# Performance work log

Measured on AMD Instinct MI355X. Metric: run time of the kernel, lower is better.

## Reference

```python
import jax, jax.numpy as jnp
import numpy as np

N_HEAD = 16
N_EMBED = 2048


def setup_inputs() -> dict:
    key = jax.random.key(0)
    k1, k2, k3, k4, k5 = jax.random.split(key, 5)
    B, T, C = 4, 2048, N_EMBED
    scale = 1.0 / np.sqrt(C)
    return {
        "x": jax.random.normal(k1, (B, T, C), dtype=jnp.float32),
        "w_attn": jax.random.normal(k2, (C, 3 * C), dtype=jnp.float32) * scale,
        "b_attn": jnp.zeros((3 * C,), dtype=jnp.float32),
        "w_proj": jax.random.normal(k3, (C, C), dtype=jnp.float32) * scale,
        "b_proj": jnp.zeros((C,), dtype=jnp.float32),
    }


def reference(x, w_attn, b_attn, w_proj, b_proj):
    B, T, C = x.shape
    H = N_HEAD
    hd = C // H
    # fused QKV projection: [B,T,3C]
    qkv = jnp.einsum("btc,cd->btd", x, w_attn) + b_attn
    q, k, v = jnp.split(qkv, 3, axis=-1)
    # [B,H,T,hd]
    q = q.reshape(B, T, H, hd).transpose(0, 2, 1, 3)
    k = k.reshape(B, T, H, hd).transpose(0, 2, 1, 3)
    v = v.reshape(B, T, H, hd).transpose(0, 2, 1, 3)
    # scaled dot-product attention (no mask, no dropout at eval)
    scores = jnp.einsum("bhqd,bhkd->bhqk", q, k) / jnp.sqrt(jnp.asarray(hd, dtype=q.dtype))
    attn = jax.nn.softmax(scores, axis=-1)
    y = jnp.einsum("bhqk,bhkd->bhqd", attn, v)
    y = y.transpose(0, 2, 1, 3).reshape(B, T, C)
    return jnp.einsum("btc,cd->btd", y, w_proj) + b_proj
```

## Files before the change

kernel.cpp:

```cpp
#include <hip/hip_runtime.h>
#include <hip/hip_fp16.h>

typedef _Float16 f16;
typedef _Float16 half8 __attribute__((ext_vector_type(8)));
typedef _Float16 half4v __attribute__((ext_vector_type(4)));
typedef float f32x4 __attribute__((ext_vector_type(4)));

#define NBAT 4
#define NT   2048
#define NC   2048
#define NHEAD 16
#define HD   128
#define NM   8192
#define N3C  6144
#define QK_LD 4096
#define ATT_SCALE 0.088388347648318447f

static __device__ __forceinline__ void gload16(const void* g, void* l) {
  __builtin_amdgcn_global_load_lds(
      (const __attribute__((address_space(1))) unsigned int*)g,
      (__attribute__((address_space(3))) unsigned int*)l, 16, 0, 0);
}


__global__ __launch_bounds__(256) void cvt_x_f16(const float* __restrict__ in,
                                                 f16* __restrict__ out) {
  size_t i = ((size_t)blockIdx.x * 256 + threadIdx.x) * 8;
  float4 a = *(const float4*)(in + i);
  float4 b = *(const float4*)(in + i + 4);
  half8 o;
  o[0] = (f16)a.x; o[1] = (f16)a.y; o[2] = (f16)a.z; o[3] = (f16)a.w;
  o[4] = (f16)b.x; o[5] = (f16)b.y; o[6] = (f16)b.z; o[7] = (f16)b.w;
  *(half8*)(out + i) = o;
}

__global__ __launch_bounds__(256) void cvt_tr_f16(const float* __restrict__ in,
                                                  f16* __restrict__ out,
                                                  int R, int CC) {
  __shared__ float tile[32][33];
  int cb = blockIdx.x * 32, rb = blockIdx.y * 32;
  int lx = threadIdx.x & 31, ly = threadIdx.x >> 5;
  for (int i = 0; i < 32; i += 8)
    tile[ly + i][lx] = in[(size_t)(rb + ly + i) * CC + cb + lx];
  __syncthreads();
  for (int i = 0; i < 32; i += 8)
    out[(size_t)(cb + ly + i) * R + rb + lx] = (f16)tile[lx][ly + i];
}

template <int OUTMODE>
__global__ __launch_bounds__(512, 2)
void gemm256(const f16* __restrict__ A, const f16* __restrict__ BT,
             const float* __restrict__ bias,
             f16* __restrict__ oqk, f16* __restrict__ ovT,
             float* __restrict__ of32, int N, int K, int nbn) {
  __shared__ f16 sA[4 * 8192];
  __shared__ f16 sB[4 * 8192];

  const int tid = threadIdx.x;
  const int wv = tid >> 6, lane = tid & 63;
  const int lr = lane & 15, lg = lane >> 4;
  const int wm = wv >> 2, wn = wv & 3;

  const int bid = blockIdx.x;
  const int xcd = bid & 7, li = bid >> 3;
  const int bm = (xcd & 3) * 8 + (li & 7);
  const int bn = (xcd >> 2) * (nbn >> 1) + (li >> 3);

  const int q0 = tid >> 3;
  const int cx = (tid & 7) ^ (q0 & 7);
  const f16* aSrc = A + (size_t)(bm * 256 + q0) * K + cx * 8;
  const f16* bSrc = BT + (size_t)(bn * 256 + q0) * K + cx * 8;
  const size_t rs64 = (size_t)64 * K, rs128 = (size_t)128 * K;

  const int NKT = K >> 6, NIT = NKT >> 1;
  f32x4 acc[8][4] = {};

  auto stgA = [&](int t, int h, int bu) {
    const f16* s = aSrc + (size_t)h * rs128 + t * 64;
    f16* d = sA + (bu * 2 + h) * 8192 + tid * 8;
    gload16(s, d);
    gload16(s + rs64, d + 4096);
  };
  auto stgB = [&](int t, int h, int bu) {
    const f16* s = bSrc + (size_t)h * rs128 + t * 64;
    f16* d = sB + (bu * 2 + h) * 8192 + tid * 8;
    gload16(s, d);
    gload16(s + rs64, d + 4096);
  };

  stgA(0, 0, 0); stgA(0, 1, 0);
  stgB(0, 0, 0); stgB(0, 1, 0);
  stgB(1, 0, 1); stgB(1, 1, 1);
  asm volatile("s_waitcnt vmcnt(4)" ::: "memory");
  __builtin_amdgcn_s_barrier();
  asm volatile("" ::: "memory");

  const int xcs[2] = {((0 * 4 + lg) ^ (lr & 7)) * 8, ((1 * 4 + lg) ^ (lr & 7)) * 8};

  for (int it = 0; it < NIT; ++it) {
    const int u = 2 * it, v = u + 1;
    const bool notlast = (it < NIT - 1);
    half8 bfrag[4][2];
#pragma unroll
    for (int p = 0; p < 8; ++p) {
      const int buf = (p < 4) ? 0 : 1;
      const f16* bA = sA + (buf * 2 + wm) * 8192;
      const f16* bB = sB + (buf * 2 + (wn >> 1)) * 8192;
      const int mf0 = (p & 3) * 2;
      if ((p & 3) == 0) {
#pragma unroll
        for (int nf = 0; nf < 4; ++nf)
#pragma unroll
          for (int ks = 0; ks < 2; ++ks)
            bfrag[nf][ks] = *(const half8*)(
                bB + ((wn & 1) * 64 + nf * 16 + lr) * 64 + xcs[ks]);
      }
      half8 afrag[2][2];
#pragma unroll
      for (int m2 = 0; m2 < 2; ++m2)
#pragma unroll
        for (int ks = 0; ks < 2; ++ks)
          afrag[m2][ks] = *(const half8*)(
              bA + ((mf0 + m2) * 16 + lr) * 64 + xcs[ks]);
      switch (p) {
        case 0: stgA(v, 0, 1); break;
        case 1: stgA(v, 1, 1); break;
        case 2: if (notlast) stgB(u + 2, 0, 0); break;
        case 3: if (notlast) stgB(u + 2, 1, 0); break;
        case 4: if (notlast) stgA(u + 2, 0, 0); break;
        case 5: if (notlast) stgA(u + 2, 1, 0); break;
        case 6: if (notlast) stgB(v + 2, 0, 1); break;
        case 7: if (notlast) stgB(v + 2, 1, 1); break;
      }
      if ((p & 3) == 3) {
        if (notlast) asm volatile("s_waitcnt vmcnt(4)" ::: "memory");
        else         asm volatile("s_waitcnt vmcnt(0)" ::: "memory");
      }
      asm volatile("" ::: "memory");
      __builtin_amdgcn_s_barrier();
      asm volatile("" ::: "memory");
      __builtin_amdgcn_s_setprio(1);
#pragma unroll
      for (int m2 = 0; m2 < 2; ++m2)
#pragma unroll
        for (int nf = 0; nf < 4; ++nf)
#pragma unroll
          for (int ks = 0; ks < 2; ++ks)
            acc[mf0 + m2][nf] = __builtin_amdgcn_mfma_f32_16x16x32_f16(
                afrag[m2][ks], bfrag[nf][ks], acc[mf0 + m2][nf], 0, 0, 0);
      __builtin_amdgcn_s_setprio(0);
      asm volatile("" ::: "memory");
      __builtin_amdgcn_s_barrier();
    }
  }

#pragma unroll
  for (int nf = 0; nf < 4; ++nf) {
    const int col = bn * 256 + wn * 64 + nf * 16 + lr;
    const float bv = bias[col];
#pragma unroll
    for (int mf = 0; mf < 8; ++mf) {
      const int row0 = bm * 256 + wm * 128 + mf * 16 + lg * 4;
      f32x4 v = acc[mf][nf];
      if (OUTMODE == 0) {
#pragma unroll
        for (int r = 0; r < 4; ++r)
          of32[(size_t)(row0 + r) * N + col] = v[r] + bv;
      } else {
        if (col < 4096) {
          const float sc = (col < 2048) ? ATT_SCALE : 1.0f;
#pragma unroll
          for (int r = 0; r < 4; ++r)
            oqk[(size_t)(row0 + r) * QK_LD + col] = (f16)((v[r] + bv) * sc);
        } else {
          const int dfull = col - 4096;
          const int hh = dfull >> 7, dd = dfull & 127;
          const int bb = row0 >> 11, tt0 = row0 & 2047;
          half4v pk;
#pragma unroll
          for (int r = 0; r < 4; ++r) pk[r] = (f16)(v[r] + bv);
          *(half4v*)(ovT + ((size_t)(bb * NHEAD + hh) * HD + dd) * NT + tt0) = pk;
        }
      }
    }
  }
}

__global__ __launch_bounds__(256, 2)
void attn_fwd(const f16* __restrict__ qk, const f16* __restrict__ vT,
              f16* __restrict__ y) {
  const int bid = blockIdx.x;
  const int sid = (bid & 7) * 128 + (bid >> 3);
  const int qt = sid & 15;
  const int bh = sid >> 4;
  const int b = bh >> 4, h = bh & 15;
  const int tid = threadIdx.x, w = tid >> 6, lane = tid & 63;
  const int lr = lane & 15, lg = lane >> 4;

  __shared__ f16 Ks[2][64 * 128];
  __shared__ f16 Vs[2][128 * 64];
  __shared__ f16 Ps[4][2][16 * 64];

  half8 qf[2][4];
  for (int s = 0; s < 2; ++s) {
    const f16* qp = qk + (size_t)(b * NT + qt * 128 + w * 32 + s * 16 + lr) * QK_LD +
                    h * HD + lg * 8;
    for (int dc = 0; dc < 4; ++dc) qf[s][dc] = *(const half8*)(qp + dc * 32);
  }

  f32x4 accy[2][8] = {};
  f32x4 lacc[2] = {};
  float mrow[2][4];
  for (int s = 0; s < 2; ++s)
    for (int r = 0; r < 4; ++r) mrow[s][r] = -1e30f;

  half8 onev;
  for (int j = 0; j < 8; ++j) onev[j] = (f16)1.0f;

  const char* kbase[4];
  const char* vbase[4];
  for (int j = 0; j < 4; ++j) {
    int idx = w * 4 + j;
    {
      int row = idx * 4 + lg;
      int swz = (lr * 16) ^ ((row & 7) << 4);
      kbase[j] = (const char*)qk +
                 ((size_t)(b * NT + row) * QK_LD + 2048 + h * HD) * 2 + swz;
    }
    {
      int d = idx * 8 + (lane >> 3);
      int cj = (lane & 7) ^ (d & 7);
      vbase[j] = (const char*)vT + ((size_t)(bh * HD + d) * NT + cj * 8) * 2;
    }
  }

  for (int j = 0; j < 4; ++j) {
    int idx = w * 4 + j;
    gload16(kbase[j], (void*)((char*)Ks[0] + idx * 1024));
    gload16(vbase[j], (void*)((char*)Vs[0] + idx * 1024));
  }

  int cur = 0;
  for (int kt = 0; kt < 32; ++kt) {
    if (kt + 1 < 32) {
      for (int j = 0; j < 4; ++j) {
        int idx = w * 4 + j;
        gload16(kbase[j] + (size_t)(kt + 1) * (64 * QK_LD * 2),
                (void*)((char*)Ks[cur ^ 1] + idx * 1024));
        gload16(vbase[j] + (size_t)(kt + 1) * 128,
                (void*)((char*)Vs[cur ^ 1] + idx * 1024));
      }
    }
    if (kt < 31) asm volatile("s_waitcnt vmcnt(8)" ::: "memory");
    else         asm volatile("s_waitcnt vmcnt(0)" ::: "memory");
    __builtin_amdgcn_s_barrier();
    asm volatile("" ::: "memory");

    f32x4 sa[2][4] = {};
    for (int nb = 0; nb < 4; ++nb) {
      int kvr = nb * 16 + lr;
      const char* kr = (const char*)Ks[cur] + kvr * 256;
      int s7 = (kvr & 7) << 4;
      for (int dc = 0; dc < 4; ++dc) {
        half8 kb = *(const half8*)(kr + ((dc * 64 + lg * 16) ^ s7));
        sa[0][nb] = __builtin_amdgcn_mfma_f32_16x16x32_f16(qf[0][dc], kb, sa[0][nb], 0, 0, 0);
        sa[1][nb] = __builtin_amdgcn_mfma_f32_16x16x32_f16(qf[1][dc], kb, sa[1][nb], 0, 0, 0);
      }
    }

    for (int s = 0; s < 2; ++s) {
      float pml[4] = {-1e30f, -1e30f, -1e30f, -1e30f};
      for (int nb = 0; nb < 4; ++nb)
        for (int r = 0; r < 4; ++r)
          pml[r] = fmaxf(pml[r], sa[s][nb][r]);
      bool ok = true;
      for (int r = 0; r < 4; ++r) ok &= (pml[r] <= mrow[s][r] + 8.0f);
      if (!__all(ok)) {
        for (int r = 0; r < 4; ++r) {
          for (int off = 1; off < 16; off <<= 1)
            pml[r] = fmaxf(pml[r], __shfl_xor(pml[r], off));
          float mn = fmaxf(mrow[s][r], pml[r]);
          float al = __expf(mrow[s][r] - mn);
          mrow[s][r] = mn;
          lacc[s][r] *= al;
          for (int db = 0; db < 8; ++db) accy[s][db][r] *= al;
        }
      }
      for (int nb = 0; nb < 4; ++nb)
        for (int r = 0; r < 4; ++r) {
          float p = __expf(sa[s][nb][r] - mrow[s][r]);
          int prow = lg * 4 + r;
          int chunk = (nb * 2 + (lr >> 3)) ^ (prow & 7);
          Ps[w][s][prow * 64 + chunk * 8 + (lr & 7)] = (f16)p;
        }
    }

    half8 pa[2][2];
    for (int s = 0; s < 2; ++s)
      for (int kc = 0; kc < 2; ++kc) {
        int chunk = (kc * 4 + lg) ^ (lr & 7);
        pa[s][kc] = *(const half8*)(&Ps[w][s][lr * 64 + chunk * 8]);
      }
    for (int s = 0; s < 2; ++s)
      for (int kc = 0; kc < 2; ++kc)
        lacc[s] = __builtin_amdgcn_mfma_f32_16x16x32_f16(pa[s][kc], onev, lacc[s], 0, 0, 0);

    for (int db = 0; db < 8; ++db) {
      int d = db * 16 + lr;
      const char* vr = (const char*)Vs[cur] + d * 128;
      int d7 = d & 7;
      for (int kc = 0; kc < 2; ++kc) {
        half8 vb = *(const half8*)(vr + (((kc * 4 + lg) ^ d7) * 16));
        accy[0][db] = __builtin_amdgcn_mfma_f32_16x16x32_f16(pa[0][kc], vb, accy[0][db], 0, 0, 0);
        accy[1][db] = __builtin_amdgcn_mfma_f32_16x16x32_f16(pa[1][kc], vb, accy[1][db], 0, 0, 0);
      }
    }

    asm volatile("" ::: "memory");
    __builtin_amdgcn_s_barrier();
    cur ^= 1;
  }

  for (int s = 0; s < 2; ++s) {
    f32x4 inv;
    for (int r = 0; r < 4; ++r) inv[r] = 1.0f / lacc[s][r];
    f16* yp = y + (size_t)(b * NT + qt * 128 + w * 32 + s * 16 + lg * 4) * NC +
              h * HD + lr;
    for (int db = 0; db < 8; ++db)
      for (int r = 0; r < 4; ++r)
        yp[(size_t)r * NC + db * 16] = (f16)(accy[s][db][r] * inv[r]);
  }
}

extern "C" void kernel_launch(void* const* d_in, const int* in_sizes, int n_in,
                              void* d_out, int out_size, void* d_ws, size_t ws_size,
                              hipStream_t stream) {
  (void)in_sizes; (void)n_in; (void)out_size; (void)ws_size;
  const float* x      = (const float*)d_in[0];
  const float* w_attn = (const float*)d_in[1];
  const float* b_attn = (const float*)d_in[2];
  const float* w_proj = (const float*)d_in[3];
  const float* b_proj = (const float*)d_in[4];
  float* out = (float*)d_out;

  char* p = (char*)d_ws;
  f16* xh  = (f16*)p; p += (size_t)NM * NC * 2;
  f16* waT = (f16*)p; p += (size_t)N3C * NC * 2;
  f16* wpT = (f16*)p; p += (size_t)NC * NC * 2;
  f16* qkb = (f16*)p; p += (size_t)NM * QK_LD * 2;
  f16* vT  = (f16*)p; p += (size_t)NBAT * NHEAD * HD * NT * 2;
  f16* yh  = (f16*)p; p += (size_t)NM * NC * 2;

  cvt_x_f16<<<8192, 256, 0, stream>>>(x, xh);
  cvt_tr_f16<<<dim3(192, 64), 256, 0, stream>>>(w_attn, waT, NC, N3C);
  cvt_tr_f16<<<dim3(64, 64), 256, 0, stream>>>(w_proj, wpT, NC, NC);
  gemm256<1><<<768, 512, 0, stream>>>(xh, waT, b_attn, qkb, vT, nullptr,
                                      N3C, NC, 24);
  attn_fwd<<<1024, 256, 0, stream>>>(qkb, vT, yh);
  gemm256<0><<<256, 512, 0, stream>>>(yh, wpT, b_proj, nullptr, nullptr,
                                      out, NC, NC, 8);
}
```

Baseline: 472.8 us.

## Double-buffer LDS fragment reads in GEMM and reorder attention MFMA loops

The GEMM main loop is rewritten so that LDS reads for the next A/B fragment group are issued into a second register set while the MFMAs for the current group run. This hides LDS latency behind matrix math. Launch bounds are relaxed to one block per CU to make room for the extra fragment registers, which may cost occupancy. The attention kernel's QK and PV loops are reordered so the k-chunk index is outermost, interleaving independent accumulator chains.

```diff
diff --git a/kernel.cpp b/kernel.cpp
--- a/kernel.cpp
+++ b/kernel.cpp
@@ -48,7 +48,7 @@
 }
 
 template <int OUTMODE>
-__global__ __launch_bounds__(512, 2)
+__global__ __launch_bounds__(512, 1)
 void gemm256(const f16* __restrict__ A, const f16* __restrict__ BT,
              const float* __restrict__ bias,
              f16* __restrict__ oqk, f16* __restrict__ ovT,
@@ -96,63 +96,99 @@
   asm volatile("" ::: "memory");
 
   const int xcs[2] = {((0 * 4 + lg) ^ (lr & 7)) * 8, ((1 * 4 + lg) ^ (lr & 7)) * 8};
+  const f16* bAbase = sA + wm * 8192;
+  const f16* bBbase = sB + (wn >> 1) * 8192 + ((wn & 1) * 64 + lr) * 64;
+
+  half8 af0[2][2], af1[2][2];
+  half8 bf0[4][2], bf1[4][2];
+
+#define RD_A(DST, BUF, MQ)                                                  \
+  {                                                                         \
+    const f16* _pa = bAbase + (BUF)*16384;                                  \
+    _Pragma("unroll") for (int m2 = 0; m2 < 2; ++m2)                        \
+      _Pragma("unroll") for (int ks = 0; ks < 2; ++ks)                      \
+        DST[m2][ks] = *(const half8*)(_pa + (((MQ) + m2) * 16 + lr) * 64 +  \
+                                      xcs[ks]);                             \
+  }
+#define RD_B(DST, BUF)                                                      \
+  {                                                                         \
+    const f16* _pb = bBbase + (BUF)*16384;                                  \
+    _Pragma("unroll") for (int nf = 0; nf < 4; ++nf)                        \
+      _Pragma("unroll") for (int ks = 0; ks < 2; ++ks)                      \
+        DST[nf][ks] = *(const half8*)(_pb + nf * 16 * 64 + xcs[ks]);        \
+  }
+#define MFMA16(AF, BF, MF0)                                                 \
+  __builtin_amdgcn_s_setprio(1);                                            \
+  _Pragma("unroll") for (int ks = 0; ks < 2; ++ks)                          \
+    _Pragma("unroll") for (int m2 = 0; m2 < 2; ++m2)                        \
+      _Pragma("unroll") for (int nf = 0; nf < 4; ++nf)                      \
+        acc[(MF0) + m2][nf] = __builtin_amdgcn_mfma_f32_16x16x32_f16(       \
+            AF[m2][ks], BF[nf][ks], acc[(MF0) + m2][nf], 0, 0, 0);          \
+  __builtin_amdgcn_s_setprio(0);
+#define BAR1 asm volatile("" ::: "memory"); __builtin_amdgcn_s_barrier(); \
+             asm volatile("" ::: "memory");
+#define BAR2 asm volatile("" ::: "memory"); __builtin_amdgcn_s_barrier();
+
+  RD_A(af0, 0, 0);
+  RD_B(bf0, 0);
 
   for (int it = 0; it < NIT; ++it) {
     const int u = 2 * it, v = u + 1;
     const bool notlast = (it < NIT - 1);
-    half8 bfrag[4][2];
-#pragma unroll
-    for (int p = 0; p < 8; ++p) {
-      const int buf = (p < 4) ? 0 : 1;
-      const f16* bA = sA + (buf * 2 + wm) * 8192;
-      const f16* bB = sB + (buf * 2 + (wn >> 1)) * 8192;
-      const int mf0 = (p & 3) * 2;
-      if ((p & 3) == 0) {
-#pragma unroll
-        for (int nf = 0; nf < 4; ++nf)
-#pragma unroll
-          for (int ks = 0; ks < 2; ++ks)
-            bfrag[nf][ks] = *(const half8*)(
-                bB + ((wn & 1) * 64 + nf * 16 + lr) * 64 + xcs[ks]);
-      }
-      half8 afrag[2][2];
-#pragma unroll
-      for (int m2 = 0; m2 < 2; ++m2)
-#pragma unroll
-        for (int ks = 0; ks < 2; ++ks)
-          afrag[m2][ks] = *(const half8*)(
-              bA + ((mf0 + m2) * 16 + lr) * 64 + xcs[ks]);
-      switch (p) {
-        case 0: stgA(v, 0, 1); break;
-        case 1: stgA(v, 1, 1); break;
-        case 2: if (notlast) stgB(u + 2, 0, 0); break;
-        case 3: if (notlast) stgB(u + 2, 1, 0); break;
-        case 4: if (notlast) stgA(u + 2, 0, 0); break;
-        case 5: if (notlast) stgA(u + 2, 1, 0); break;
-        case 6: if (notlast) stgB(v + 2, 0, 1); break;
-        case 7: if (notlast) stgB(v + 2, 1, 1); break;
-      }
-      if ((p & 3) == 3) {
-        if (notlast) asm volatile("s_waitcnt vmcnt(4)" ::: "memory");
-        else         asm volatile("s_waitcnt vmcnt(0)" ::: "memory");
-      }
-      asm volatile("" ::: "memory");
-      __builtin_amdgcn_s_barrier();
-      asm volatile("" ::: "memory");
-      __builtin_amdgcn_s_setprio(1);
-#pragma unroll
-      for (int m2 = 0; m2 < 2; ++m2)
-#pragma unroll
-        for (int nf = 0; nf < 4; ++nf)
-#pragma unroll
-          for (int ks = 0; ks < 2; ++ks)
-            acc[mf0 + m2][nf] = __builtin_amdgcn_mfma_f32_16x16x32_f16(
-                afrag[m2][ks], bfrag[nf][ks], acc[mf0 + m2][nf], 0, 0, 0);
-      __builtin_amdgcn_s_setprio(0);
-      asm volatile("" ::: "memory");
-      __builtin_amdgcn_s_barrier();
-    }
-  }
+    stgA(v, 0, 1);
+    BAR1;
+    RD_A(af1, 0, 2);
+    MFMA16(af0, bf0, 0);
+    BAR2;
+    stgA(v, 1, 1);
+    BAR1;
+    RD_A(af0, 0, 4);
+    MFMA16(af1, bf0, 2);
+    BAR2;
+    if (notlast) stgB(u + 2, 0, 0);
+    BAR1;
+    RD_A(af1, 0, 6);
+    MFMA16(af0, bf0, 4);
+    BAR2;
+    if (notlast) stgB(u + 2, 1, 0);
+    if (notlast) { asm volatile("s_waitcnt vmcnt(4)" ::: "memory"); }
+    else         { asm volatile("s_waitcnt vmcnt(0)" ::: "memory"); }
+    BAR1;
+    RD_A(af0, 1, 0);
+    RD_B(bf1, 1);
+    MFMA16(af1, bf0, 6);
+    BAR2;
+    if (notlast) stgA(u + 2, 0, 0);
+    BAR1;
+    RD_A(af1, 1, 2);
+    MFMA16(af0, bf1, 0);
+    BAR2;
+    if (notlast) stgA(u + 2, 1, 0);
+    BAR1;
+    RD_A(af0, 1, 4);
+    MFMA16(af1, bf1, 2);
+    BAR2;
+    if (notlast) stgB(v + 2, 0, 1);
+    BAR1;
+    RD_A(af1, 1, 6);
+    MFMA16(af0, bf1, 4);
+    BAR2;
+    if (notlast) stgB(v + 2, 1, 1);
+    if (notlast) { asm volatile("s_waitcnt vmcnt(4)" ::: "memory"); }
+    else         { asm volatile("s_waitcnt vmcnt(0)" ::: "memory"); }
+    BAR1;
+    if (notlast) {
+      RD_A(af0, 0, 0);
+      RD_B(bf0, 0);
+    }
+    MFMA16(af1, bf1, 6);
+    BAR2;
+  }
+#undef RD_A
+#undef RD_B
+#undef MFMA16
+#undef BAR1
+#undef BAR2
 
 #pragma unroll
   for (int nf = 0; nf < 4; ++nf) {
@@ -161,24 +197,24 @@
 #pragma unroll
     for (int mf = 0; mf < 8; ++mf) {
       const int row0 = bm * 256 + wm * 128 + mf * 16 + lg * 4;
-      f32x4 v = acc[mf][nf];
+      f32x4 vv = acc[mf][nf];
       if (OUTMODE == 0) {
 #pragma unroll
         for (int r = 0; r < 4; ++r)
-          of32[(size_t)(row0 + r) * N + col] = v[r] + bv;
+          of32[(size_t)(row0 + r) * N + col] = vv[r] + bv;
       } else {
         if (col < 4096) {
           const float sc = (col < 2048) ? ATT_SCALE : 1.0f;
 #pragma unroll
           for (int r = 0; r < 4; ++r)
-            oqk[(size_t)(row0 + r) * QK_LD + col] = (f16)((v[r] + bv) * sc);
+            oqk[(size_t)(row0 + r) * QK_LD + col] = (f16)((vv[r] + bv) * sc);
         } else {
           const int dfull = col - 4096;
           const int hh = dfull >> 7, dd = dfull & 127;
           const int bb = row0 >> 11, tt0 = row0 & 2047;
           half4v pk;
 #pragma unroll
-          for (int r = 0; r < 4; ++r) pk[r] = (f16)(v[r] + bv);
+          for (int r = 0; r < 4; ++r) pk[r] = (f16)(vv[r] + bv);
           *(half4v*)(ovT + ((size_t)(bb * NHEAD + hh) * HD + dd) * NT + tt0) = pk;
         }
       }
@@ -257,11 +293,13 @@
     asm volatile("" ::: "memory");
 
     f32x4 sa[2][4] = {};
-    for (int nb = 0; nb < 4; ++nb) {
-      int kvr = nb * 16 + lr;
-      const char* kr = (const char*)Ks[cur] + kvr * 256;
-      int s7 = (kvr & 7) << 4;
-      for (int dc = 0; dc < 4; ++dc) {
+#pragma unroll
+    for (int dc = 0; dc < 4; ++dc) {
+#pragma unroll
+      for (int nb = 0; nb < 4; ++nb) {
+        int kvr = nb * 16 + lr;
+        const char* kr = (const char*)Ks[cur] + kvr * 256;
+        int s7 = (kvr & 7) << 4;
         half8 kb = *(const half8*)(kr + ((dc * 64 + lg * 16) ^ s7));
         sa[0][nb] = __builtin_amdgcn_mfma_f32_16x16x32_f16(qf[0][dc], kb, sa[0][nb], 0, 0, 0);
         sa[1][nb] = __builtin_amdgcn_mfma_f32_16x16x32_f16(qf[1][dc], kb, sa[1][nb], 0, 0, 0);
@@ -301,15 +339,19 @@
         int chunk = (kc * 4 + lg) ^ (lr & 7);
         pa[s][kc] = *(const half8*)(&Ps[w][s][lr * 64 + chunk * 8]);
       }
-    for (int s = 0; s < 2; ++s)
-      for (int kc = 0; kc < 2; ++kc)
+#pragma unroll
+    for (int kc = 0; kc < 2; ++kc)
+#pragma unroll
+      for (int s = 0; s < 2; ++s)
         lacc[s] = __builtin_amdgcn_mfma_f32_16x16x32_f16(pa[s][kc], onev, lacc[s], 0, 0, 0);
 
-    for (int db = 0; db < 8; ++db) {
-      int d = db * 16 + lr;
-      const char* vr = (const char*)Vs[cur] + d * 128;
-      int d7 = d & 7;
-      for (int kc = 0; kc < 2; ++kc) {
+#pragma unroll
+    for (int kc = 0; kc < 2; ++kc) {
+#pragma unroll
+      for (int db = 0; db < 8; ++db) {
+        int d = db * 16 + lr;
+        const char* vr = (const char*)Vs[cur] + d * 128;
+        int d7 = d & 7;
         half8 vb = *(const half8*)(vr + (((kc * 4 + lg) ^ d7) * 16));
         accy[0][db] = __builtin_amdgcn_mfma_f32_16x16x32_f16(pa[0][kc], vb, accy[0][db], 0, 0, 0);
         accy[1][db] = __builtin_amdgcn_mfma_f32_16x16x32_f16(pa[1][kc], vb, accy[1][db], 0, 0, 0);
```

New measurement: 726.5 us. 53.6% more time.
